# Kernel optimization log

Hardware: AMD Instinct MI355X
Metric: run time of the kernel (lower is better)

## Reference

```python
import jax, jax.numpy as jnp
import numpy as np
import math

NUM_HEADS = 16
KEY_DIM = 64
MODEL_DIM = 1024
NEG_INF = -1000000000.0


def _get_slopes(n):
    def pow2_slopes(n):
        start = 2 ** (-2 ** (-(math.log2(n) - 3)))
        return [start * start ** i for i in range(n)]
    if math.log2(n).is_integer():
        s = pow2_slopes(n)
    else:
        c = 2 ** math.floor(math.log2(n))
        s = pow2_slopes(c) + pow2_slopes(2 * c)[0::2][: n - c]
    return jnp.asarray(s, dtype=jnp.float32)


def setup_inputs() -> dict:
    key = jax.random.key(0)
    ks = jax.random.split(key, 11)
    B, S, D = 4, 2048, MODEL_DIM
    P = NUM_HEADS * KEY_DIM
    sd = 1.0 / math.sqrt(D)
    return {
        "query": jax.random.normal(ks[0], (B, S, D), jnp.float32),
        "key": jax.random.normal(ks[1], (B, S, D), jnp.float32),
        "value": jax.random.normal(ks[2], (B, S, D), jnp.float32),
        "Wq": jax.random.normal(ks[3], (D, P), jnp.float32) * sd,
        "bq": jnp.zeros((P,), jnp.float32),
        "Wk": jax.random.normal(ks[4], (D, P), jnp.float32) * sd,
        "bk": jnp.zeros((P,), jnp.float32),
        "Wv": jax.random.normal(ks[5], (D, P), jnp.float32) * sd,
        "bv": jnp.zeros((P,), jnp.float32),
        "Wo": jax.random.normal(ks[6], (P, D), jnp.float32) * (1.0 / math.sqrt(P)),
        "bo": jnp.zeros((D,), jnp.float32),
    }


def reference(query, key, value, Wq, bq, Wk, bk, Wv, bv, Wo, bo):
    B, S, _ = query.shape
    H, Kd = NUM_HEADS, KEY_DIM

    def split_heads(x):  # [B,S,H*Kd] -> [B,H,S,Kd]
        return x.reshape(B, S, H, Kd).transpose(0, 2, 1, 3)

    q = split_heads(query @ Wq + bq)
    k = split_heads(key @ Wk + bk)
    v = split_heads(value @ Wv + bv)

    logits = jnp.einsum("bhqd,bhkd->bhqk", q, k) / jnp.sqrt(jnp.float32(Kd))

    i = jnp.arange(S)[:, None]
    j = jnp.arange(S)[None, :]
    causal = jnp.where(i >= j, 0.0, NEG_INF).astype(jnp.float32)  # [S,S]
    rel = (i - j).astype(jnp.float32)  # [S,S]
    slopes = _get_slopes(H)  # [H]
    alibi = slopes[:, None, None] * rel  # [H,S,S]
    logits = logits + causal[None, None, :, :] + alibi[None, :, :, :]

    weights = jax.nn.softmax(logits, axis=-1)
    attn = jnp.einsum("bhqk,bhkd->bhqd", weights, v)
    concat = attn.transpose(0, 2, 1, 3).reshape(B, S, H * Kd)
    return concat @ Wo + bo
```

## Files before the change

kernel.cpp:

```cpp
#include <hip/hip_runtime.h>

#define B_ 4
#define S_ 2048
#define D_ 1024
#define H_ 16
#define KD_ 64
#define P_ 1024
#define M_ (B_*S_)

typedef unsigned short u16;
typedef unsigned int u32;
typedef __attribute__((ext_vector_type(2))) unsigned u32x2;
typedef __attribute__((ext_vector_type(4))) float f32x4;
typedef __attribute__((ext_vector_type(8))) __bf16 bf16x8;

__device__ __forceinline__ u16 f2bf(float f) {
  u32 x = __float_as_uint(f);
  return (u16)((x + 0x7fffu + ((x >> 16) & 1u)) >> 16);
}

__device__ __forceinline__ void gl_lds16(const u16* g, u16* l) {
  __builtin_amdgcn_global_load_lds((__attribute__((address_space(1))) void*)g,
                                   (__attribute__((address_space(3))) void*)l, 16, 0, 0);
}

__device__ __forceinline__ u32 pkbf(float a, float b) {
  return __builtin_amdgcn_perm(__float_as_uint(b) + 0x8000u,
                               __float_as_uint(a) + 0x8000u, 0x07060302u);
}

#if __has_builtin(__builtin_amdgcn_permlane32_swap) && __has_builtin(__builtin_amdgcn_permlane16_swap)
__device__ __forceinline__ void plswap(u32& a, u32& b) {
  u32x2 r32 = __builtin_amdgcn_permlane32_swap(a, b, false, false);
  u32x2 r16 = __builtin_amdgcn_permlane16_swap(r32[0], r32[1], false, false);
  a = r16[0]; b = r16[1];
}
#else
__device__ __forceinline__ void plswap(u32& a, u32& b) {
  const int l = threadIdx.x & 63;
  const int quad = l >> 4, l16 = l & 15;
  int i0 = (((quad & 1) * 32) + l16) * 4;
  int i1 = i0 + 64;
  int a_lo = __builtin_amdgcn_ds_bpermute(i0, (int)a);
  int b_lo = __builtin_amdgcn_ds_bpermute(i0, (int)b);
  int a_hi = __builtin_amdgcn_ds_bpermute(i1, (int)a);
  int b_hi = __builtin_amdgcn_ds_bpermute(i1, (int)b);
  u32 na = (quad < 2) ? (u32)a_lo : (u32)b_lo;
  u32 nb = (quad < 2) ? (u32)a_hi : (u32)b_hi;
  a = na; b = nb;
}
#endif

__global__ void cvt3_kernel(const float* __restrict__ q, const float* __restrict__ k,
                            const float* __restrict__ v,
                            u16* __restrict__ Xq, u16* __restrict__ Xk, u16* __restrict__ Xv) {
  const int z = blockIdx.y;
  const float* in = z == 0 ? q : z == 1 ? k : v;
  u16* out = z == 0 ? Xq : z == 1 ? Xk : Xv;
  int i = blockIdx.x * 256 + threadIdx.x;
  float4 vv = ((const float4*)in)[i];
  ((u32*)out)[i*2+0] = (u32)f2bf(vv.x) | ((u32)f2bf(vv.y) << 16);
  ((u32*)out)[i*2+1] = (u32)f2bf(vv.z) | ((u32)f2bf(vv.w) << 16);
}

__global__ void transpose_cvt4(const float* __restrict__ Wq, const float* __restrict__ Wk,
                               const float* __restrict__ Wv, const float* __restrict__ Wo,
                               u16* __restrict__ WqT, u16* __restrict__ WkT,
                               u16* __restrict__ WvT, u16* __restrict__ WoT) {
  const int z = blockIdx.z;
  const float* in = z == 0 ? Wq : z == 1 ? Wk : z == 2 ? Wv : Wo;
  u16* out = z == 0 ? WqT : z == 1 ? WkT : z == 2 ? WvT : WoT;
  __shared__ float tile[32][33];
  int bx = blockIdx.x * 32, by = blockIdx.y * 32;
  int tx = threadIdx.x, ty = threadIdx.y;
  #pragma unroll
  for (int kk = 0; kk < 4; ++kk)
    tile[ty + kk*8][tx] = in[(by + ty + kk*8) * 1024 + bx + tx];
  __syncthreads();
  #pragma unroll
  for (int kk = 0; kk < 4; ++kk)
    out[(bx + ty + kk*8) * 1024 + by + tx] = f2bf(tile[tx][ty + kk*8]);
}

__global__ __launch_bounds__(256) void gemm_qkv(
    const u16* __restrict__ Xq, const u16* __restrict__ Xk, const u16* __restrict__ Xv,
    const u16* __restrict__ WqT, const u16* __restrict__ WkT, const u16* __restrict__ WvT,
    const float* __restrict__ bq, const float* __restrict__ bk, const float* __restrict__ bv,
    u16* __restrict__ Qb, u16* __restrict__ Kb, u16* __restrict__ Vt)
{
  constexpr int K = 1024, N = 1024, BK = 32;
  const int z = blockIdx.z;
  const u16* A  = z == 0 ? Xq  : z == 1 ? Xk  : Xv;
  const u16* Bt = z == 0 ? WqT : z == 1 ? WkT : WvT;
  const float* bias = z == 0 ? bq : z == 1 ? bk : bv;

  __shared__ alignas(16) u16 As[128*BK];
  __shared__ alignas(16) u16 Bs[128*BK];
  const int tid = threadIdx.x;
  const int w = tid >> 6, l = tid & 63;
  const int quad = l >> 4, l16 = l & 15;
  const int wm = (w >> 1) * 64, wn = (w & 1) * 64;
  const long mBase = (long)blockIdx.x * 128;
  const int  nBase = blockIdx.y * 128;

  f32x4 acc[4][4] = {};
  const int off0 = w*1024 + l*16;

  for (int kb = 0; kb < K/BK; ++kb) {
    __syncthreads();
    #pragma unroll
    for (int p = 0; p < 2; ++p) {
      int off = p*4096 + off0;
      int row = off >> 6;
      int cb  = off & 63;
      const u16* ga = A  + (mBase + row)*K + kb*BK + (cb >> 1);
      const u16* gb = Bt + ((long)(nBase + row))*K + kb*BK + (cb >> 1);
      gl_lds16(ga, (u16*)((char*)As + p*4096 + w*1024));
      gl_lds16(gb, (u16*)((char*)Bs + p*4096 + w*1024));
    }
    __syncthreads();
    bf16x8 af[4], bf[4];
    #pragma unroll
    for (int i = 0; i < 4; ++i) af[i] = *(const bf16x8*)&As[(wm + i*16 + l16)*BK + quad*8];
    #pragma unroll
    for (int j = 0; j < 4; ++j) bf[j] = *(const bf16x8*)&Bs[(wn + j*16 + l16)*BK + quad*8];
    #pragma unroll
    for (int i = 0; i < 4; ++i)
      #pragma unroll
      for (int j = 0; j < 4; ++j)
        acc[i][j] = __builtin_amdgcn_mfma_f32_16x16x32_bf16(af[i], bf[j], acc[i][j], 0, 0, 0);
  }

  if (z < 2) {
    u16* Cout = z == 0 ? Qb : Kb;
    #pragma unroll
    for (int i = 0; i < 4; ++i)
      #pragma unroll
      for (int j = 0; j < 4; ++j)
        #pragma unroll
        for (int r = 0; r < 4; ++r) {
          long row = mBase + wm + i*16 + quad*4 + r;
          int  col = nBase + wn + j*16 + l16;
          Cout[row*N + col] = f2bf(acc[i][j][r] + bias[col]);
        }
  } else {
    #pragma unroll
    for (int i = 0; i < 4; ++i)
      #pragma unroll
      for (int j = 0; j < 4; ++j) {
        int  col  = nBase + wn + j*16 + l16;
        long row0 = mBase + wm + i*16 + quad*4;
        int  bb = (int)(row0 >> 11);
        int  ss = (int)(row0 & 2047);
        float bcol = bias[col];
        float v0 = acc[i][j][0] + bcol, v1 = acc[i][j][1] + bcol;
        float v2 = acc[i][j][2] + bcol, v3 = acc[i][j][3] + bcol;
        uint2 pk;
        pk.x = (u32)f2bf(v0) | ((u32)f2bf(v1) << 16);
        pk.y = (u32)f2bf(v2) | ((u32)f2bf(v3) << 16);
        *(uint2*)&Vt[((long)(bb*16) * 64 + col) * 2048 + ss] = pk;
      }
  }
}

__global__ __launch_bounds__(256) void gemm_out(const u16* __restrict__ A,
                                                const u16* __restrict__ Bt,
                                                const float* __restrict__ bias,
                                                float* __restrict__ Cout)
{
  constexpr int K = 1024, N = 1024, BK = 32;
  __shared__ alignas(16) u16 As[128*BK];
  __shared__ alignas(16) u16 Bs[128*BK];
  const int tid = threadIdx.x;
  const int w = tid >> 6, l = tid & 63;
  const int quad = l >> 4, l16 = l & 15;
  const int wm = (w >> 1) * 64, wn = (w & 1) * 64;
  const long mBase = (long)blockIdx.x * 128;
  const int  nBase = blockIdx.y * 128;

  f32x4 acc[4][4] = {};
  const int off0 = w*1024 + l*16;

  for (int kb = 0; kb < K/BK; ++kb) {
    __syncthreads();
    #pragma unroll
    for (int p = 0; p < 2; ++p) {
      int off = p*4096 + off0;
      int row = off >> 6;
      int cb  = off & 63;
      const u16* ga = A  + (mBase + row)*K + kb*BK + (cb >> 1);
      const u16* gb = Bt + ((long)(nBase + row))*K + kb*BK + (cb >> 1);
      gl_lds16(ga, (u16*)((char*)As + p*4096 + w*1024));
      gl_lds16(gb, (u16*)((char*)Bs + p*4096 + w*1024));
    }
    __syncthreads();
    bf16x8 af[4], bf[4];
    #pragma unroll
    for (int i = 0; i < 4; ++i) af[i] = *(const bf16x8*)&As[(wm + i*16 + l16)*BK + quad*8];
    #pragma unroll
    for (int j = 0; j < 4; ++j) bf[j] = *(const bf16x8*)&Bs[(wn + j*16 + l16)*BK + quad*8];
    #pragma unroll
    for (int i = 0; i < 4; ++i)
      #pragma unroll
      for (int j = 0; j < 4; ++j)
        acc[i][j] = __builtin_amdgcn_mfma_f32_16x16x32_bf16(af[i], bf[j], acc[i][j], 0, 0, 0);
  }

  #pragma unroll
  for (int i = 0; i < 4; ++i)
    #pragma unroll
    for (int j = 0; j < 4; ++j)
      #pragma unroll
      for (int r = 0; r < 4; ++r) {
        long row = mBase + wm + i*16 + quad*4 + r;
        int  col = nBase + wn + j*16 + l16;
        Cout[row*N + col] = acc[i][j][r] + bias[col];
      }
}

__global__ __launch_bounds__(256, 2) void attn_kernel(const u16* __restrict__ Qb,
                                                      const u16* __restrict__ Kb,
                                                      const u16* __restrict__ Vt,
                                                      u16* __restrict__ Ob)
{
  const int n = blockIdx.x;
  const int pairIdx = n >> 6;
  const int r6 = n & 63;
  const int b = r6 >> 4, h = r6 & 15;
  const int w = threadIdx.x >> 6;
  const int l = threadIdx.x & 63;
  const int quad = l >> 4, l16 = l & 15;
  const float LOG2E = 1.44269504089f;
  const float slope = exp2f(-0.5f * (float)(h + 1));
  const float c1  = 0.125f * LOG2E;
  const float sl2 = slope * LOG2E;
  const float rs1 = sl2, rs2 = 2.f*sl2, rs3 = 3.f*sl2;

  const u16* Kp = Kb + ((long)(b*S_))*P_ + h*KD_;
  const u16* Vp = Vt + ((long)(b*H_ + h))*KD_*S_;

  for (int half = 0; half < 2; ++half) {
    const int qt = half == 0 ? (15 - pairIdx) : pairIdx;
    const int q0 = qt*128 + w*32;
    const u16* Qp = Qb + ((long)(b*S_ + q0))*P_ + h*KD_;

    bf16x8 qf[2][2];
    #pragma unroll
    for (int i = 0; i < 2; ++i)
      #pragma unroll
      for (int kk = 0; kk < 2; ++kk)
        qf[i][kk] = *(const bf16x8*)&Qp[(long)(i*16 + l16)*P_ + kk*32 + quad*8];

    f32x4 o[2][4] = {};
    float lsum[2] = {0.f, 0.f};

    auto issue = [&](int it, bf16x8& k00, bf16x8& k01, bf16x8& k10, bf16x8& k11,
                     bf16x8& v0, bf16x8& v1, bf16x8& v2, bf16x8& v3) {
      const int kt = it >> 2, ks = it & 3;
      const u16* kp = Kp + (long)(kt*128 + l16 + 2*ks*16)*P_;
      k00 = *(const bf16x8*)(kp + quad*8);
      k01 = *(const bf16x8*)(kp + 32 + quad*8);
      k10 = *(const bf16x8*)(kp + 16*P_ + quad*8);
      k11 = *(const bf16x8*)(kp + 16*P_ + 32 + quad*8);
      const u16* vp = Vp + (long)l16*S_ + kt*128 + ks*32 + quad*8;
      v0 = *(const bf16x8*)(vp);
      v1 = *(const bf16x8*)(vp + 16*S_);
      v2 = *(const bf16x8*)(vp + 32*S_);
      v3 = *(const bf16x8*)(vp + 48*S_);
    };
    auto compute = [&](int it, const bf16x8& k00, const bf16x8& k01,
                       const bf16x8& k10, const bf16x8& k11,
                       const bf16x8& v0, const bf16x8& v1,
                       const bf16x8& v2, const bf16x8& v3) {
      const int kt = it >> 2, ks = it & 3;
      const float kb0 = (float)(kt*128 + 2*ks*16 + quad*4);
      u32 pw0[2][2], pw1[2][2];
      {
        const float bij = -sl2 * kb0;
        #pragma unroll
        for (int i = 0; i < 2; ++i) {
          f32x4 t = {};
          t = __builtin_amdgcn_mfma_f32_16x16x32_bf16(k00, qf[i][0], t, 0, 0, 0);
          t = __builtin_amdgcn_mfma_f32_16x16x32_bf16(k01, qf[i][1], t, 0, 0, 0);
          float p0 = __builtin_amdgcn_exp2f(fmaf(t[0], c1, bij));
          float p1 = __builtin_amdgcn_exp2f(fmaf(t[1], c1, bij) - rs1);
          float p2 = __builtin_amdgcn_exp2f(fmaf(t[2], c1, bij) - rs2);
          float p3 = __builtin_amdgcn_exp2f(fmaf(t[3], c1, bij) - rs3);
          lsum[i] += (p0 + p1) + (p2 + p3);
          pw0[i][0] = pkbf(p0, p1);
          pw0[i][1] = pkbf(p2, p3);
        }
      }
      {
        const float bij = -sl2 * (kb0 + 16.f);
        #pragma unroll
        for (int i = 0; i < 2; ++i) {
          f32x4 t = {};
          t = __builtin_amdgcn_mfma_f32_16x16x32_bf16(k10, qf[i][0], t, 0, 0, 0);
          t = __builtin_amdgcn_mfma_f32_16x16x32_bf16(k11, qf[i][1], t, 0, 0, 0);
          float p0 = __builtin_amdgcn_exp2f(fmaf(t[0], c1, bij));
          float p1 = __builtin_amdgcn_exp2f(fmaf(t[1], c1, bij) - rs1);
          float p2 = __builtin_amdgcn_exp2f(fmaf(t[2], c1, bij) - rs2);
          float p3 = __builtin_amdgcn_exp2f(fmaf(t[3], c1, bij) - rs3);
          lsum[i] += (p0 + p1) + (p2 + p3);
          pw1[i][0] = pkbf(p0, p1);
          pw1[i][1] = pkbf(p2, p3);
        }
      }
      bf16x8 pb[2];
      #pragma unroll
      for (int i = 0; i < 2; ++i) {
        u32 fa0 = pw0[i][0], fb0 = pw1[i][0];
        u32 fa1 = pw0[i][1], fb1 = pw1[i][1];
        plswap(fa0, fb0);
        plswap(fa1, fb1);
        union { u32 u[4]; bf16x8 v; } fu;
        fu.u[0] = fa0; fu.u[1] = fa1; fu.u[2] = fb0; fu.u[3] = fb1;
        pb[i] = fu.v;
      }
      o[0][0] = __builtin_amdgcn_mfma_f32_16x16x32_bf16(v0, pb[0], o[0][0], 0, 0, 0);
      o[1][0] = __builtin_amdgcn_mfma_f32_16x16x32_bf16(v0, pb[1], o[1][0], 0, 0, 0);
      o[0][1] = __builtin_amdgcn_mfma_f32_16x16x32_bf16(v1, pb[0], o[0][1], 0, 0, 0);
      o[1][1] = __builtin_amdgcn_mfma_f32_16x16x32_bf16(v1, pb[1], o[1][1], 0, 0, 0);
      o[0][2] = __builtin_amdgcn_mfma_f32_16x16x32_bf16(v2, pb[0], o[0][2], 0, 0, 0);
      o[1][2] = __builtin_amdgcn_mfma_f32_16x16x32_bf16(v2, pb[1], o[1][2], 0, 0, 0);
      o[0][3] = __builtin_amdgcn_mfma_f32_16x16x32_bf16(v3, pb[0], o[0][3], 0, 0, 0);
      o[1][3] = __builtin_amdgcn_mfma_f32_16x16x32_bf16(v3, pb[1], o[1][3], 0, 0, 0);
    };

    const int nit = qt * 4;
    if (nit > 0) {
      bf16x8 ak00, ak01, ak10, ak11, av0, av1, av2, av3;
      bf16x8 bk00, bk01, bk10, bk11, bv0, bv1, bv2, bv3;
      issue(0, ak00, ak01, ak10, ak11, av0, av1, av2, av3);
      int it = 0;
      while (true) {
        if (it + 1 < nit) issue(it + 1, bk00, bk01, bk10, bk11, bv0, bv1, bv2, bv3);
        compute(it, ak00, ak01, ak10, ak11, av0, av1, av2, av3);
        ++it; if (it == nit) break;
        if (it + 1 < nit) issue(it + 1, ak00, ak01, ak10, ak11, av0, av1, av2, av3);
        compute(it, bk00, bk01, bk10, bk11, bv0, bv1, bv2, bv3);
        ++it; if (it == nit) break;
      }
    }

    {
      const int kt = qt;
      const int ksmax = w + 1;
      const u16* kts = Kp + (long)(kt*128 + l16)*P_;
      for (int ks = 0; ks < ksmax; ++ks) {
        u32 pw[2][2][2];
        #pragma unroll
        for (int jp = 0; jp < 2; ++jp) {
          const int j = 2*ks + jp;
          const u16* kp = kts + (long)(j*16)*P_;
          bf16x8 kf0 = *(const bf16x8*)(kp + quad*8);
          bf16x8 kf1 = *(const bf16x8*)(kp + 32 + quad*8);
          const int kl0 = j*16 + quad*4;
          const float bij = -sl2 * (float)(kt*128 + kl0);
          #pragma unroll
          for (int i = 0; i < 2; ++i) {
            const int ql = w*32 + i*16 + l16;
            f32x4 t = {};
            t = __builtin_amdgcn_mfma_f32_16x16x32_bf16(kf0, qf[i][0], t, 0, 0, 0);
            t = __builtin_amdgcn_mfma_f32_16x16x32_bf16(kf1, qf[i][1], t, 0, 0, 0);
            float x0 = fmaf(t[0], c1, bij);
            float x1 = fmaf(t[1], c1, bij) - rs1;
            float x2 = fmaf(t[2], c1, bij) - rs2;
            float x3 = fmaf(t[3], c1, bij) - rs3;
            if (kl0 + 0 > ql) x0 = -1e30f;
            if (kl0 + 1 > ql) x1 = -1e30f;
            if (kl0 + 2 > ql) x2 = -1e30f;
            if (kl0 + 3 > ql) x3 = -1e30f;
            float p0 = __builtin_amdgcn_exp2f(x0);
            float p1 = __builtin_amdgcn_exp2f(x1);
            float p2 = __builtin_amdgcn_exp2f(x2);
            float p3 = __builtin_amdgcn_exp2f(x3);
            lsum[i] += (p0 + p1) + (p2 + p3);
            pw[i][jp][0] = pkbf(p0, p1);
            pw[i][jp][1] = pkbf(p2, p3);
          }
        }
        bf16x8 pb[2];
        #pragma unroll
        for (int i = 0; i < 2; ++i) {
          u32 fa0 = pw[i][0][0], fb0 = pw[i][1][0];
          u32 fa1 = pw[i][0][1], fb1 = pw[i][1][1];
          plswap(fa0, fb0);
          plswap(fa1, fb1);
          union { u32 u[4]; bf16x8 v; } fu;
          fu.u[0] = fa0; fu.u[1] = fa1; fu.u[2] = fb0; fu.u[3] = fb1;
          pb[i] = fu.v;
        }
        #pragma unroll
        for (int jn = 0; jn < 4; ++jn) {
          bf16x8 vf = *(const bf16x8*)&Vp[(long)(jn*16 + l16)*S_ + kt*128 + ks*32 + quad*8];
          o[0][jn] = __builtin_amdgcn_mfma_f32_16x16x32_bf16(vf, pb[0], o[0][jn], 0, 0, 0);
          o[1][jn] = __builtin_amdgcn_mfma_f32_16x16x32_bf16(vf, pb[1], o[1][jn], 0, 0, 0);
        }
      }
    }

    #pragma unroll
    for (int i = 0; i < 2; ++i) {
      lsum[i] += __shfl_xor(lsum[i], 16, 64);
      lsum[i] += __shfl_xor(lsum[i], 32, 64);
      const float inv = 1.0f / lsum[i];
      #pragma unroll
      for (int jn = 0; jn < 4; ++jn) {
        float v0 = o[i][jn][0] * inv, v1 = o[i][jn][1] * inv;
        float v2 = o[i][jn][2] * inv, v3 = o[i][jn][3] * inv;
        uint2 pk;
        pk.x = (u32)f2bf(v0) | ((u32)f2bf(v1) << 16);
        pk.y = (u32)f2bf(v2) | ((u32)f2bf(v3) << 16);
        *(uint2*)&Ob[((long)(b*S_ + q0 + i*16 + l16))*P_ + h*KD_ + jn*16 + quad*4] = pk;
      }
    }
  }
}

extern "C" void kernel_launch(void* const* d_in, const int* in_sizes, int n_in,
                              void* d_out, int out_size, void* d_ws, size_t ws_size,
                              hipStream_t stream) {
  const float* q  = (const float*)d_in[0];
  const float* k  = (const float*)d_in[1];
  const float* v  = (const float*)d_in[2];
  const float* Wq = (const float*)d_in[3];
  const float* bq = (const float*)d_in[4];
  const float* Wk = (const float*)d_in[5];
  const float* bk = (const float*)d_in[6];
  const float* Wv = (const float*)d_in[7];
  const float* bv = (const float*)d_in[8];
  const float* Wo = (const float*)d_in[9];
  const float* bo = (const float*)d_in[10];

  const size_t X_ELEMS = (size_t)M_ * P_;
  const size_t W_ELEMS = (size_t)D_ * P_;
  u16* ws  = (u16*)d_ws;
  u16* Xq  = ws;
  u16* Xk  = Xq  + X_ELEMS;
  u16* Xv  = Xk  + X_ELEMS;
  u16* WqT = Xv  + X_ELEMS;
  u16* WkT = WqT + W_ELEMS;
  u16* WvT = WkT + W_ELEMS;
  u16* WoT = WvT + W_ELEMS;
  u16* Qb  = WoT + W_ELEMS;
  u16* Kb  = Qb  + X_ELEMS;
  u16* Vt  = Kb  + X_ELEMS;
  u16* Attn = Xq;

  cvt3_kernel<<<dim3((unsigned)(X_ELEMS/4/256), 3), 256, 0, stream>>>(q, k, v, Xq, Xk, Xv);

  transpose_cvt4<<<dim3(32, 32, 4), dim3(32, 8), 0, stream>>>(Wq, Wk, Wv, Wo,
                                                              WqT, WkT, WvT, WoT);

  gemm_qkv<<<dim3(M_/128, P_/128, 3), 256, 0, stream>>>(Xq, Xk, Xv, WqT, WkT, WvT,
                                                        bq, bk, bv, Qb, Kb, Vt);

  attn_kernel<<<dim3(512), 256, 0, stream>>>(Qb, Kb, Vt, Attn);

  gemm_out<<<dim3(M_/128, P_/128), 256, 0, stream>>>(Attn, WoT, bo, (float*)d_out);
}
```

Baseline: 381.2 us.

## Give each attention wave 64 query rows, one q-tile per block

```diff
diff --git a/kernel.cpp b/kernel.cpp
--- a/kernel.cpp
+++ b/kernel.cpp
@@ -218,13 +218,13 @@
       }
 }
 
-__global__ __launch_bounds__(256, 2) void attn_kernel(const u16* __restrict__ Qb,
+__global__ __launch_bounds__(128, 2) void attn_kernel(const u16* __restrict__ Qb,
                                                       const u16* __restrict__ Kb,
                                                       const u16* __restrict__ Vt,
                                                       u16* __restrict__ Ob)
 {
   const int n = blockIdx.x;
-  const int pairIdx = n >> 6;
+  const int qt = 15 - (n >> 6);
   const int r6 = n & 63;
   const int b = r6 >> 4, h = r6 & 15;
   const int w = threadIdx.x >> 6;
@@ -236,185 +236,175 @@
   const float sl2 = slope * LOG2E;
   const float rs1 = sl2, rs2 = 2.f*sl2, rs3 = 3.f*sl2;
 
+  const int q0 = qt*128 + w*64;
+  const u16* Qp = Qb + ((long)(b*S_ + q0))*P_ + h*KD_;
   const u16* Kp = Kb + ((long)(b*S_))*P_ + h*KD_;
   const u16* Vp = Vt + ((long)(b*H_ + h))*KD_*S_;
 
-  for (int half = 0; half < 2; ++half) {
-    const int qt = half == 0 ? (15 - pairIdx) : pairIdx;
-    const int q0 = qt*128 + w*32;
-    const u16* Qp = Qb + ((long)(b*S_ + q0))*P_ + h*KD_;
-
-    bf16x8 qf[2][2];
-    #pragma unroll
-    for (int i = 0; i < 2; ++i)
-      #pragma unroll
-      for (int kk = 0; kk < 2; ++kk)
-        qf[i][kk] = *(const bf16x8*)&Qp[(long)(i*16 + l16)*P_ + kk*32 + quad*8];
-
-    f32x4 o[2][4] = {};
-    float lsum[2] = {0.f, 0.f};
-
-    auto issue = [&](int it, bf16x8& k00, bf16x8& k01, bf16x8& k10, bf16x8& k11,
-                     bf16x8& v0, bf16x8& v1, bf16x8& v2, bf16x8& v3) {
-      const int kt = it >> 2, ks = it & 3;
-      const u16* kp = Kp + (long)(kt*128 + l16 + 2*ks*16)*P_;
-      k00 = *(const bf16x8*)(kp + quad*8);
-      k01 = *(const bf16x8*)(kp + 32 + quad*8);
-      k10 = *(const bf16x8*)(kp + 16*P_ + quad*8);
-      k11 = *(const bf16x8*)(kp + 16*P_ + 32 + quad*8);
+  bf16x8 qf[4][2];
+  #pragma unroll
+  for (int i = 0; i < 4; ++i)
+    #pragma unroll
+    for (int kk = 0; kk < 2; ++kk)
+      qf[i][kk] = *(const bf16x8*)&Qp[(long)(i*16 + l16)*P_ + kk*32 + quad*8];
+
+  f32x4 o[4][4] = {};
+  float lsum[4] = {0.f, 0.f, 0.f, 0.f};
+
+  auto kissue = [&](int it, bf16x8& k00, bf16x8& k01, bf16x8& k10, bf16x8& k11) {
+    const int kt = it >> 2, ks = it & 3;
+    const u16* kp = Kp + (long)(kt*128 + l16 + 2*ks*16)*P_;
+    k00 = *(const bf16x8*)(kp + quad*8);
+    k01 = *(const bf16x8*)(kp + 32 + quad*8);
+    k10 = *(const bf16x8*)(kp + 16*P_ + quad*8);
+    k11 = *(const bf16x8*)(kp + 16*P_ + 32 + quad*8);
+  };
+  auto compute = [&](int it, const bf16x8& k00, const bf16x8& k01,
+                     const bf16x8& k10, const bf16x8& k11) {
+    const int kt = it >> 2, ks = it & 3;
+    const u16* vp = Vp + (long)l16*S_ + kt*128 + ks*32 + quad*8;
+    bf16x8 v0 = *(const bf16x8*)(vp);
+    bf16x8 v1 = *(const bf16x8*)(vp + 16*S_);
+    bf16x8 v2 = *(const bf16x8*)(vp + 32*S_);
+    bf16x8 v3 = *(const bf16x8*)(vp + 48*S_);
+    const float kb0 = (float)(kt*128 + 2*ks*16 + quad*4);
+    u32 pw0[4][2], pw1[4][2];
+    {
+      const float bij = -sl2 * kb0;
+      #pragma unroll
+      for (int i = 0; i < 4; ++i) {
+        f32x4 t = {};
+        t = __builtin_amdgcn_mfma_f32_16x16x32_bf16(k00, qf[i][0], t, 0, 0, 0);
+        t = __builtin_amdgcn_mfma_f32_16x16x32_bf16(k01, qf[i][1], t, 0, 0, 0);
+        float p0 = __builtin_amdgcn_exp2f(fmaf(t[0], c1, bij));
+        float p1 = __builtin_amdgcn_exp2f(fmaf(t[1], c1, bij) - rs1);
+        float p2 = __builtin_amdgcn_exp2f(fmaf(t[2], c1, bij) - rs2);
+        float p3 = __builtin_amdgcn_exp2f(fmaf(t[3], c1, bij) - rs3);
+        lsum[i] += (p0 + p1) + (p2 + p3);
+        pw0[i][0] = pkbf(p0, p1);
+        pw0[i][1] = pkbf(p2, p3);
+      }
+    }
+    {
+      const float bij = -sl2 * (kb0 + 16.f);
+      #pragma unroll
+      for (int i = 0; i < 4; ++i) {
+        f32x4 t = {};
+        t = __builtin_amdgcn_mfma_f32_16x16x32_bf16(k10, qf[i][0], t, 0, 0, 0);
+        t = __builtin_amdgcn_mfma_f32_16x16x32_bf16(k11, qf[i][1], t, 0, 0, 0);
+        float p0 = __builtin_amdgcn_exp2f(fmaf(t[0], c1, bij));
+        float p1 = __builtin_amdgcn_exp2f(fmaf(t[1], c1, bij) - rs1);
+        float p2 = __builtin_amdgcn_exp2f(fmaf(t[2], c1, bij) - rs2);
+        float p3 = __builtin_amdgcn_exp2f(fmaf(t[3], c1, bij) - rs3);
+        lsum[i] += (p0 + p1) + (p2 + p3);
+        pw1[i][0] = pkbf(p0, p1);
+        pw1[i][1] = pkbf(p2, p3);
+      }
+    }
+    #pragma unroll
+    for (int i = 0; i < 4; ++i) {
+      u32 fa0 = pw0[i][0], fb0 = pw1[i][0];
+      u32 fa1 = pw0[i][1], fb1 = pw1[i][1];
+      plswap(fa0, fb0);
+      plswap(fa1, fb1);
+      union { u32 u[4]; bf16x8 v; } fu;
+      fu.u[0] = fa0; fu.u[1] = fa1; fu.u[2] = fb0; fu.u[3] = fb1;
+      const bf16x8 pb = fu.v;
+      o[i][0] = __builtin_amdgcn_mfma_f32_16x16x32_bf16(v0, pb, o[i][0], 0, 0, 0);
+      o[i][1] = __builtin_amdgcn_mfma_f32_16x16x32_bf16(v1, pb, o[i][1], 0, 0, 0);
+      o[i][2] = __builtin_amdgcn_mfma_f32_16x16x32_bf16(v2, pb, o[i][2], 0, 0, 0);
+      o[i][3] = __builtin_amdgcn_mfma_f32_16x16x32_bf16(v3, pb, o[i][3], 0, 0, 0);
+    }
+  };
+
+  const int nit = qt * 4;
+  if (nit > 0) {
+    bf16x8 ak00, ak01, ak10, ak11;
+    bf16x8 bk00, bk01, bk10, bk11;
+    kissue(0, ak00, ak01, ak10, ak11);
+    int it = 0;
+    while (true) {
+      if (it + 1 < nit) kissue(it + 1, bk00, bk01, bk10, bk11);
+      compute(it, ak00, ak01, ak10, ak11);
+      ++it; if (it == nit) break;
+      if (it + 1 < nit) kissue(it + 1, ak00, ak01, ak10, ak11);
+      compute(it, bk00, bk01, bk10, bk11);
+      ++it; if (it == nit) break;
+    }
+  }
+
+  {
+    const int kt = qt;
+    const int ksmax = 2*w + 2;
+    const u16* kts = Kp + (long)(kt*128 + l16)*P_;
+    for (int ks = 0; ks < ksmax; ++ks) {
       const u16* vp = Vp + (long)l16*S_ + kt*128 + ks*32 + quad*8;
-      v0 = *(const bf16x8*)(vp);
-      v1 = *(const bf16x8*)(vp + 16*S_);
-      v2 = *(const bf16x8*)(vp + 32*S_);
-      v3 = *(const bf16x8*)(vp + 48*S_);
-    };
-    auto compute = [&](int it, const bf16x8& k00, const bf16x8& k01,
-                       const bf16x8& k10, const bf16x8& k11,
-                       const bf16x8& v0, const bf16x8& v1,
-                       const bf16x8& v2, const bf16x8& v3) {
-      const int kt = it >> 2, ks = it & 3;
-      const float kb0 = (float)(kt*128 + 2*ks*16 + quad*4);
-      u32 pw0[2][2], pw1[2][2];
-      {
-        const float bij = -sl2 * kb0;
+      bf16x8 v0 = *(const bf16x8*)(vp);
+      bf16x8 v1 = *(const bf16x8*)(vp + 16*S_);
+      bf16x8 v2 = *(const bf16x8*)(vp + 32*S_);
+      bf16x8 v3 = *(const bf16x8*)(vp + 48*S_);
+      u32 pw[4][2][2];
+      #pragma unroll
+      for (int jp = 0; jp < 2; ++jp) {
+        const int j = 2*ks + jp;
+        const u16* kp = kts + (long)(j*16)*P_;
+        bf16x8 kf0 = *(const bf16x8*)(kp + quad*8);
+        bf16x8 kf1 = *(const bf16x8*)(kp + 32 + quad*8);
+        const int kl0 = j*16 + quad*4;
+        const float bij = -sl2 * (float)(kt*128 + kl0);
         #pragma unroll
-        for (int i = 0; i < 2; ++i) {
+        for (int i = 0; i < 4; ++i) {
+          const int ql = w*64 + i*16 + l16;
           f32x4 t = {};
-          t = __builtin_amdgcn_mfma_f32_16x16x32_bf16(k00, qf[i][0], t, 0, 0, 0);
-          t = __builtin_amdgcn_mfma_f32_16x16x32_bf16(k01, qf[i][1], t, 0, 0, 0);
-          float p0 = __builtin_amdgcn_exp2f(fmaf(t[0], c1, bij));
-          float p1 = __builtin_amdgcn_exp2f(fmaf(t[1], c1, bij) - rs1);
-          float p2 = __builtin_amdgcn_exp2f(fmaf(t[2], c1, bij) - rs2);
-          float p3 = __builtin_amdgcn_exp2f(fmaf(t[3], c1, bij) - rs3);
+          t = __builtin_amdgcn_mfma_f32_16x16x32_bf16(kf0, qf[i][0], t, 0, 0, 0);
+          t = __builtin_amdgcn_mfma_f32_16x16x32_bf16(kf1, qf[i][1], t, 0, 0, 0);
+          float x0 = fmaf(t[0], c1, bij);
+          float x1 = fmaf(t[1], c1, bij) - rs1;
+          float x2 = fmaf(t[2], c1, bij) - rs2;
+          float x3 = fmaf(t[3], c1, bij) - rs3;
+          if (kl0 + 0 > ql) x0 = -1e30f;
+          if (kl0 + 1 > ql) x1 = -1e30f;
+          if (kl0 + 2 > ql) x2 = -1e30f;
+          if (kl0 + 3 > ql) x3 = -1e30f;
+          float p0 = __builtin_amdgcn_exp2f(x0);
+          float p1 = __builtin_amdgcn_exp2f(x1);
+          float p2 = __builtin_amdgcn_exp2f(x2);
+          float p3 = __builtin_amdgcn_exp2f(x3);
           lsum[i] += (p0 + p1) + (p2 + p3);
-          pw0[i][0] = pkbf(p0, p1);
-          pw0[i][1] = pkbf(p2, p3);
+          pw[i][jp][0] = pkbf(p0, p1);
+          pw[i][jp][1] = pkbf(p2, p3);
         }
       }
-      {
-        const float bij = -sl2 * (kb0 + 16.f);
-        #pragma unroll
-        for (int i = 0; i < 2; ++i) {
-          f32x4 t = {};
-          t = __builtin_amdgcn_mfma_f32_16x16x32_bf16(k10, qf[i][0], t, 0, 0, 0);
-          t = __builtin_amdgcn_mfma_f32_16x16x32_bf16(k11, qf[i][1], t, 0, 0, 0);
-          float p0 = __builtin_amdgcn_exp2f(fmaf(t[0], c1, bij));
-          float p1 = __builtin_amdgcn_exp2f(fmaf(t[1], c1, bij) - rs1);
-          float p2 = __builtin_amdgcn_exp2f(fmaf(t[2], c1, bij) - rs2);
-          float p3 = __builtin_amdgcn_exp2f(fmaf(t[3], c1, bij) - rs3);
-          lsum[i] += (p0 + p1) + (p2 + p3);
-          pw1[i][0] = pkbf(p0, p1);
-          pw1[i][1] = pkbf(p2, p3);
-        }
-      }
-      bf16x8 pb[2];
-      #pragma unroll
-      for (int i = 0; i < 2; ++i) {
-        u32 fa0 = pw0[i][0], fb0 = pw1[i][0];
-        u32 fa1 = pw0[i][1], fb1 = pw1[i][1];
+      #pragma unroll
+      for (int i = 0; i < 4; ++i) {
+        u32 fa0 = pw[i][0][0], fb0 = pw[i][1][0];
+        u32 fa1 = pw[i][0][1], fb1 = pw[i][1][1];
         plswap(fa0, fb0);
         plswap(fa1, fb1);
         union { u32 u[4]; bf16x8 v; } fu;
         fu.u[0] = fa0; fu.u[1] = fa1; fu.u[2] = fb0; fu.u[3] = fb1;
-        pb[i] = fu.v;
-      }
-      o[0][0] = __builtin_amdgcn_mfma_f32_16x16x32_bf16(v0, pb[0], o[0][0], 0, 0, 0);
-      o[1][0] = __builtin_amdgcn_mfma_f32_16x16x32_bf16(v0, pb[1], o[1][0], 0, 0, 0);
-      o[0][1] = __builtin_amdgcn_mfma_f32_16x16x32_bf16(v1, pb[0], o[0][1], 0, 0, 0);
-      o[1][1] = __builtin_amdgcn_mfma_f32_16x16x32_bf16(v1, pb[1], o[1][1], 0, 0, 0);
-      o[0][2] = __builtin_amdgcn_mfma_f32_16x16x32_bf16(v2, pb[0], o[0][2], 0, 0, 0);
-      o[1][2] = __builtin_amdgcn_mfma_f32_16x16x32_bf16(v2, pb[1], o[1][2], 0, 0, 0);
-      o[0][3] = __builtin_amdgcn_mfma_f32_16x16x32_bf16(v3, pb[0], o[0][3], 0, 0, 0);
-      o[1][3] = __builtin_amdgcn_mfma_f32_16x16x32_bf16(v3, pb[1], o[1][3], 0, 0, 0);
-    };
-
-    const int nit = qt * 4;
-    if (nit > 0) {
-      bf16x8 ak00, ak01, ak10, ak11, av0, av1, av2, av3;
-      bf16x8 bk00, bk01, bk10, bk11, bv0, bv1, bv2, bv3;
-      issue(0, ak00, ak01, ak10, ak11, av0, av1, av2, av3);
-      int it = 0;
-      while (true) {
-        if (it + 1 < nit) issue(it + 1, bk00, bk01, bk10, bk11, bv0, bv1, bv2, bv3);
-        compute(it, ak00, ak01, ak10, ak11, av0, av1, av2, av3);
-        ++it; if (it == nit) break;
-        if (it + 1 < nit) issue(it + 1, ak00, ak01, ak10, ak11, av0, av1, av2, av3);
-        compute(it, bk00, bk01, bk10, bk11, bv0, bv1, bv2, bv3);
-        ++it; if (it == nit) break;
-      }
-    }
-
-    {
-      const int kt = qt;
-      const int ksmax = w + 1;
-      const u16* kts = Kp + (long)(kt*128 + l16)*P_;
-      for (int ks = 0; ks < ksmax; ++ks) {
-        u32 pw[2][2][2];
-        #pragma unroll
-        for (int jp = 0; jp < 2; ++jp) {
-          const int j = 2*ks + jp;
-          const u16* kp = kts + (long)(j*16)*P_;
-          bf16x8 kf0 = *(const bf16x8*)(kp + quad*8);
-          bf16x8 kf1 = *(const bf16x8*)(kp + 32 + quad*8);
-          const int kl0 = j*16 + quad*4;
-          const float bij = -sl2 * (float)(kt*128 + kl0);
-          #pragma unroll
-          for (int i = 0; i < 2; ++i) {
-            const int ql = w*32 + i*16 + l16;
-            f32x4 t = {};
-            t = __builtin_amdgcn_mfma_f32_16x16x32_bf16(kf0, qf[i][0], t, 0, 0, 0);
-            t = __builtin_amdgcn_mfma_f32_16x16x32_bf16(kf1, qf[i][1], t, 0, 0, 0);
-            float x0 = fmaf(t[0], c1, bij);
-            float x1 = fmaf(t[1], c1, bij) - rs1;
-            float x2 = fmaf(t[2], c1, bij) - rs2;
-            float x3 = fmaf(t[3], c1, bij) - rs3;
-            if (kl0 + 0 > ql) x0 = -1e30f;
-            if (kl0 + 1 > ql) x1 = -1e30f;
-            if (kl0 + 2 > ql) x2 = -1e30f;
-            if (kl0 + 3 > ql) x3 = -1e30f;
-            float p0 = __builtin_amdgcn_exp2f(x0);
-            float p1 = __builtin_amdgcn_exp2f(x1);
-            float p2 = __builtin_amdgcn_exp2f(x2);
-            float p3 = __builtin_amdgcn_exp2f(x3);
-            lsum[i] += (p0 + p1) + (p2 + p3);
-            pw[i][jp][0] = pkbf(p0, p1);
-            pw[i][jp][1] = pkbf(p2, p3);
-          }
-        }
-        bf16x8 pb[2];
-        #pragma unroll
-        for (int i = 0; i < 2; ++i) {
-          u32 fa0 = pw[i][0][0], fb0 = pw[i][1][0];
-          u32 fa1 = pw[i][0][1], fb1 = pw[i][1][1];
-          plswap(fa0, fb0);
-          plswap(fa1, fb1);
-          union { u32 u[4]; bf16x8 v; } fu;
-          fu.u[0] = fa0; fu.u[1] = fa1; fu.u[2] = fb0; fu.u[3] = fb1;
-          pb[i] = fu.v;
-        }
-        #pragma unroll
-        for (int jn = 0; jn < 4; ++jn) {
-          bf16x8 vf = *(const bf16x8*)&Vp[(long)(jn*16 + l16)*S_ + kt*128 + ks*32 + quad*8];
-          o[0][jn] = __builtin_amdgcn_mfma_f32_16x16x32_bf16(vf, pb[0], o[0][jn], 0, 0, 0);
-          o[1][jn] = __builtin_amdgcn_mfma_f32_16x16x32_bf16(vf, pb[1], o[1][jn], 0, 0, 0);
-        }
-      }
-    }
-
-    #pragma unroll
-    for (int i = 0; i < 2; ++i) {
-      lsum[i] += __shfl_xor(lsum[i], 16, 64);
-      lsum[i] += __shfl_xor(lsum[i], 32, 64);
-      const float inv = 1.0f / lsum[i];
-      #pragma unroll
-      for (int jn = 0; jn < 4; ++jn) {
-        float v0 = o[i][jn][0] * inv, v1 = o[i][jn][1] * inv;
-        float v2 = o[i][jn][2] * inv, v3 = o[i][jn][3] * inv;
-        uint2 pk;
-        pk.x = (u32)f2bf(v0) | ((u32)f2bf(v1) << 16);
-        pk.y = (u32)f2bf(v2) | ((u32)f2bf(v3) << 16);
-        *(uint2*)&Ob[((long)(b*S_ + q0 + i*16 + l16))*P_ + h*KD_ + jn*16 + quad*4] = pk;
-      }
+        const bf16x8 pb = fu.v;
+        o[i][0] = __builtin_amdgcn_mfma_f32_16x16x32_bf16(v0, pb, o[i][0], 0, 0, 0);
+        o[i][1] = __builtin_amdgcn_mfma_f32_16x16x32_bf16(v1, pb, o[i][1], 0, 0, 0);
+        o[i][2] = __builtin_amdgcn_mfma_f32_16x16x32_bf16(v2, pb, o[i][2], 0, 0, 0);
+        o[i][3] = __builtin_amdgcn_mfma_f32_16x16x32_bf16(v3, pb, o[i][3], 0, 0, 0);
+      }
+    }
+  }
+
+  #pragma unroll
+  for (int i = 0; i < 4; ++i) {
+    lsum[i] += __shfl_xor(lsum[i], 16, 64);
+    lsum[i] += __shfl_xor(lsum[i], 32, 64);
+    const float inv = 1.0f / lsum[i];
+    #pragma unroll
+    for (int jn = 0; jn < 4; ++jn) {
+      float v0 = o[i][jn][0] * inv, v1 = o[i][jn][1] * inv;
+      float v2 = o[i][jn][2] * inv, v3 = o[i][jn][3] * inv;
+      uint2 pk;
+      pk.x = (u32)f2bf(v0) | ((u32)f2bf(v1) << 16);
+      pk.y = (u32)f2bf(v2) | ((u32)f2bf(v3) << 16);
+      *(uint2*)&Ob[((long)(b*S_ + q0 + i*16 + l16))*P_ + h*KD_ + jn*16 + quad*4] = pk;
     }
   }
 }
@@ -457,7 +447,7 @@
   gemm_qkv<<<dim3(M_/128, P_/128, 3), 256, 0, stream>>>(Xq, Xk, Xv, WqT, WkT, WvT,
                                                         bq, bk, bv, Qb, Kb, Vt);
 
-  attn_kernel<<<dim3(512), 256, 0, stream>>>(Qb, Kb, Vt, Attn);
+  attn_kernel<<<dim3(1024), 128, 0, stream>>>(Qb, Kb, Vt, Attn);
 
   gemm_out<<<dim3(M_/128, P_/128), 256, 0, stream>>>(Attn, WoT, bo, (float*)d_out);
 }
```

After: 341.0 us. -10.5%, faster.
